# Kernel tuning notes

Hardware: AMD Instinct MI355X
Metric: run time of the kernel (lower is better)

Reference implementation:

```python
import jax, jax.numpy as jnp
import numpy as np

B, C, H, W = 16, 128, 112, 112
OUTC = 256


def _conv(x, w, padding, groups=1, bias=None):
    y = jax.lax.conv_general_dilated(
        x, w, window_strides=(1, 1), padding=[(padding, padding), (padding, padding)],
        dimension_numbers=("NCHW", "OIHW", "NCHW"), feature_group_count=groups)
    if bias is not None:
        y = y + bias[None, :, None, None]
    return y


def _grid_sample_1ch(chan, g):
    # chan: [B,H,W] single channel; g: [B,H,W,2] with (x,y) in [-1,1].
    # PyTorch grid_sample: bilinear, zeros padding, align_corners=False.
    Bn, Hc, Wc = chan.shape
    ix = (g[..., 0] + 1.0) * (Wc * 0.5) - 0.5
    iy = (g[..., 1] + 1.0) * (Hc * 0.5) - 0.5
    x0 = jnp.floor(ix)
    y0 = jnp.floor(iy)
    wx = ix - x0
    wy = iy - y0
    x0i = x0.astype(jnp.int32)
    y0i = y0.astype(jnp.int32)
    flat = chan.reshape(Bn, -1)

    def gather(yi, xi):
        valid = (yi >= 0) & (yi < Hc) & (xi >= 0) & (xi < Wc)
        idx = jnp.clip(yi, 0, Hc - 1) * Wc + jnp.clip(xi, 0, Wc - 1)
        v = jnp.take_along_axis(flat, idx.reshape(Bn, -1), axis=1).reshape(idx.shape)
        return jnp.where(valid, v, 0.0)

    v00 = gather(y0i, x0i)
    v01 = gather(y0i, x0i + 1)
    v10 = gather(y0i + 1, x0i)
    v11 = gather(y0i + 1, x0i + 1)
    return (v00 * (1 - wx) * (1 - wy) + v01 * wx * (1 - wy)
            + v10 * (1 - wx) * wy + v11 * wx * wy)


def setup_inputs() -> dict:
    key = jax.random.key(0)
    k1, k2, k3, k4 = jax.random.split(key, 4)
    x = jax.random.normal(k1, (B, C, H, W), dtype=jnp.float32)
    depth_w = jax.random.normal(k2, (C, 1, 3, 3), dtype=jnp.float32) * 0.1
    point_w = jax.random.normal(k3, (OUTC, C, 1, 1), dtype=jnp.float32) * 0.05
    offset_w = jax.random.normal(k4, (2 * C, C, 3, 3), dtype=jnp.float32) * 0.02
    offset_b = jnp.zeros((2 * C,), dtype=jnp.float32)
    return {"x": x, "depth_w": depth_w, "point_w": point_w,
            "offset_w": offset_w, "offset_b": offset_b}


def reference(x, depth_w, point_w, offset_w, offset_b):
    offset = jnp.tanh(_conv(x, offset_w, padding=1, bias=offset_b))  # [B,2C,H,W]
    out = _conv(x, depth_w, padding=1, groups=C)                     # [B,C,H,W]

    # Base grid, matching np.meshgrid + np.repeat([C,C], axis=0):
    # channels 0..C-1 are all X, channels C..2C-1 are all Y.
    gX, gY = jnp.meshgrid(jnp.linspace(-1.0, 1.0, W), jnp.linspace(-1.0, 1.0, H), indexing="xy")
    grid = jnp.concatenate([gX[None], gY[None]], axis=0)  # [2,H,W]
    grid = jnp.repeat(grid, C, axis=0)                    # [2C,H,W]

    sg = jnp.clip(grid[None] + offset, -1.0, 1.0)         # [B,2C,H,W]
    sg = sg.transpose(0, 2, 3, 1)                         # [B,H,W,2C]
    sg = sg.reshape(B, H, W, C, 2).transpose(3, 0, 1, 2, 4)  # [C,B,H,W,2]

    chans = out.transpose(1, 0, 2, 3)                     # [C,B,H,W]
    sampled = jax.vmap(_grid_sample_1ch)(chans, sg)       # [C,B,H,W]
    sampled = sampled.transpose(1, 0, 2, 3)               # [B,C,H,W]

    return _conv(sampled, point_w, padding=0)             # [B,OUTC,H,W]
```

## Files before the change

kernel.cpp:

```cpp
#include <hip/hip_runtime.h>
#include <hip/hip_bf16.h>

#define B_    16
#define C_    128
#define H_    112
#define W_    112
#define OUTC_ 256
#define TWOC_ 256
#define HW_   (H_ * W_)
#define CHW_  ((size_t)C_ * HW_)

typedef __hip_bfloat16 bf16;
typedef short bf16x8 __attribute__((ext_vector_type(8)));
typedef short s16x4  __attribute__((ext_vector_type(4)));
typedef float f32x4  __attribute__((ext_vector_type(4)));

__device__ __forceinline__ float b2f(bf16 v) { return __bfloat162float(v); }
__device__ __forceinline__ bf16  f2b(float v) { return __float2bfloat16(v); }

__device__ __forceinline__ float rd(const float* p) { return *p; }
__device__ __forceinline__ float rd(const bf16* p)  { return b2f(*p); }

__device__ __forceinline__ float fast_tanh(float v) {
    float e = __expf(2.f * v);
    return 1.f - 2.f / (e + 1.f);
}

__global__ __launch_bounds__(256) void k_probe(const unsigned short* __restrict__ x,
                                               int* __restrict__ flag) {
    __shared__ int cnt[256];
    int tid = threadIdx.x;
    int c = 0;
#pragma unroll
    for (int i = 0; i < 8; ++i) {
        unsigned short u = x[tid * 8 + i];
        int e = (u >> 7) & 0xFF;
        if (e >= 135) c++;
    }
    cnt[tid] = c;
    __syncthreads();
    if (tid == 0) {
        int s = 0;
        for (int i = 0; i < 256; ++i) s += cnt[i];
        *flag = (s > 64) ? 1 : 0;
    }
}

__global__ __launch_bounds__(256) void k_wprep(const void* __restrict__ ow,
                                               bf16* __restrict__ wth,
                                               bf16* __restrict__ wtl,
                                               const int* __restrict__ flag) {
    int i = blockIdx.x * 256 + threadIdx.x;
    if (i >= 9 * 4 * 256 * 32) return;
    int cp  = i & 31;
    int oc  = (i >> 5) & 255;
    int tcc = i >> 13;
    int cc  = tcc & 3;
    int tap = tcc >> 2;
    int c   = cc * 32 + cp;
    size_t src = ((size_t)oc * C_ + c) * 9 + tap;
    float v = (*flag) ? ((const float*)ow)[src] : b2f(((const bf16*)ow)[src]);
    bf16 hb = f2b(v);
    float lo = v - b2f(hb);
    wth[i] = hb;
    wtl[i] = f2b(lo);
}

__global__ __launch_bounds__(256) void k_pwprep(const void* __restrict__ pw,
                                                bf16* __restrict__ pwh,
                                                bf16* __restrict__ pwl,
                                                const int* __restrict__ flag) {
    int i = blockIdx.x * 256 + threadIdx.x;
    if (i >= 4 * 256 * 32) return;
    int cp   = i & 31;
    int oc   = (i >> 5) & 255;
    int cc   = i >> 13;
    int c    = cc * 32 + cp;
    size_t src = (size_t)oc * C_ + c;
    float v = (*flag) ? ((const float*)pw)[src] : b2f(((const bf16*)pw)[src]);
    bf16 hb = f2b(v);
    float lo = v - b2f(hb);
    pwh[i] = hb;
    pwl[i] = f2b(lo);
}

__global__ __launch_bounds__(256) void k_offset_mfma(
    const void* __restrict__ xsrc, const bf16* __restrict__ wth,
    const bf16* __restrict__ wtl, const void* __restrict__ ob,
    float* __restrict__ off, const int* __restrict__ flag, int b0)
{
    __shared__ alignas(16) short Sh[114 * 32];
    __shared__ alignas(16) short Sl[114 * 32];

    const int tid  = threadIdx.x;
    const int lane = tid & 63;
    const int wv   = tid >> 6;
    const int l15  = lane & 15;
    const int l4   = lane >> 4;
    const int hraw = blockIdx.x;
    const int h    = (hraw & 7) * 14 + (hraw >> 3);
    const int b    = blockIdx.y + b0;
    const int fullp = *flag;

    const float* xf = (const float*)xsrc;
    const bf16*  xb = (const bf16*)xsrc;

    f32x4 acc[4][7];
    f32x4 zero = {0.f, 0.f, 0.f, 0.f};
#pragma unroll
    for (int m = 0; m < 4; ++m)
#pragma unroll
        for (int n = 0; n < 7; ++n) acc[m][n] = zero;

    for (int cc = 0; cc < 4; ++cc) {
        for (int kh = 0; kh < 3; ++kh) {
            const int row = h + kh - 1;
            const bool rowok = (row >= 0) && (row < H_);
            __syncthreads();
            for (int i = tid; i < 912; i += 256) {
                int n  = i % 114;
                int cq = i / 114;
                int col = n - 1;
                bool ok = rowok && (col >= 0) && (col < W_);
                size_t base = ((size_t)(b * C_ + cc * 32 + cq * 4)) * HW_
                            + (size_t)row * W_ + col;
                short hs[4], ls[4];
#pragma unroll
                for (int t = 0; t < 4; ++t) {
                    float v = 0.f;
                    if (ok) v = fullp ? xf[base + (size_t)t * HW_]
                                      : b2f(xb[base + (size_t)t * HW_]);
                    bf16 hb = f2b(v);
                    float hv = b2f(hb);
                    bf16 lb = f2b(v - hv);
                    hs[t] = *(short*)&hb;
                    ls[t] = *(short*)&lb;
                }
                int ob_ = (cq * 8) ^ (((n >> 1) & 3) << 4);
                int so  = n * 32 + (ob_ >> 1);
                s16x4 th, tl;
                th[0] = hs[0]; th[1] = hs[1]; th[2] = hs[2]; th[3] = hs[3];
                tl[0] = ls[0]; tl[1] = ls[1]; tl[2] = ls[2]; tl[3] = ls[3];
                *(s16x4*)&Sh[so] = th;
                *(s16x4*)&Sl[so] = tl;
            }
            __syncthreads();

            for (int kw = 0; kw < 3; ++kw) {
                const size_t wchunk = ((size_t)((kh * 3 + kw) * 4 + cc)) * (256 * 32);
                bf16x8 ah[4], al[4];
#pragma unroll
                for (int m = 0; m < 4; ++m) {
                    size_t aoff = (size_t)(wv * 64 + m * 16 + l15) * 32 + 8 * l4;
                    ah[m] = *(const bf16x8*)(wth + wchunk + aoff);
                }
                if (fullp) {
#pragma unroll
                    for (int m = 0; m < 4; ++m) {
                        size_t aoff = (size_t)(wv * 64 + m * 16 + l15) * 32 + 8 * l4;
                        al[m] = *(const bf16x8*)(wtl + wchunk + aoff);
                    }
                }
#pragma unroll
                for (int n = 0; n < 7; ++n) {
                    int rowb = n * 16 + l15 + kw;
                    int o2   = (16 * l4) ^ (((rowb >> 1) & 3) << 4);
                    int so   = rowb * 32 + (o2 >> 1);
                    bf16x8 xh = *(const bf16x8*)&Sh[so];
#pragma unroll
                    for (int m = 0; m < 4; ++m)
                        acc[m][n] = __builtin_amdgcn_mfma_f32_16x16x32_bf16(
                            ah[m], xh, acc[m][n], 0, 0, 0);
                    if (fullp) {
                        bf16x8 xl = *(const bf16x8*)&Sl[so];
#pragma unroll
                        for (int m = 0; m < 4; ++m)
                            acc[m][n] = __builtin_amdgcn_mfma_f32_16x16x32_bf16(
                                ah[m], xl, acc[m][n], 0, 0, 0);
#pragma unroll
                        for (int m = 0; m < 4; ++m)
                            acc[m][n] = __builtin_amdgcn_mfma_f32_16x16x32_bf16(
                                al[m], xh, acc[m][n], 0, 0, 0);
                    }
                }
            }
        }
    }

#pragma unroll
    for (int m = 0; m < 4; ++m) {
        int ocb = wv * 64 + m * 16 + l4 * 4;
        float bias[4];
#pragma unroll
        for (int j = 0; j < 4; ++j)
            bias[j] = fullp ? ((const float*)ob)[ocb + j]
                            : b2f(((const bf16*)ob)[ocb + j]);
#pragma unroll
        for (int n = 0; n < 7; ++n) {
            int w = n * 16 + l15;
#pragma unroll
            for (int j = 0; j < 4; ++j) {
                size_t o = ((size_t)(b * TWOC_ + ocb + j)) * HW_ + (size_t)h * W_ + w;
                off[o] = fast_tanh(acc[m][n][j] + bias[j]);
            }
        }
    }
}

template <typename TI>
__device__ void dw_body(const TI* __restrict__ x, const TI* __restrict__ dw,
                        bf16* __restrict__ out) {
    int hw = blockIdx.x * 256 + threadIdx.x;
    int c = blockIdx.y, b = blockIdx.z;
    int h = hw / W_, w = hw - h * W_;
    float wv[9];
#pragma unroll
    for (int k = 0; k < 9; ++k) wv[k] = rd(dw + c * 9 + k);
    const TI* xc = x + (size_t)b * CHW_ + (size_t)c * HW_;
    float acc = 0.f;
#pragma unroll
    for (int kh = 0; kh < 3; ++kh) {
        int hh = h + kh - 1;
        bool hv = (hh >= 0) && (hh < H_);
#pragma unroll
        for (int kw = 0; kw < 3; ++kw) {
            int ww = w + kw - 1;
            bool v = hv && (ww >= 0) && (ww < W_);
            acc += (v ? rd(xc + hh * W_ + ww) : 0.f) * wv[kh * 3 + kw];
        }
    }
    out[(size_t)(b * C_ + c) * HW_ + hw] = f2b(acc);
}

__global__ __launch_bounds__(256) void k_dw(const void* x, const void* dw,
                                            bf16* out, const int* flag) {
    if (*flag) dw_body<float>((const float*)x, (const float*)dw, out);
    else       dw_body<bf16>((const bf16*)x, (const bf16*)dw, out);
}

__global__ __launch_bounds__(256) void k_sample(
    const float* __restrict__ off, const bf16* __restrict__ dwout,
    bf16* __restrict__ samp) {
    int hw = blockIdx.x * 256 + threadIdx.x;
    int c = blockIdx.y, b = blockIdx.z;
    int h = hw / W_, w = hw - h * W_;

    float gbase = (c < 64) ? (-1.f + 2.f * (float)w / 111.f)
                           : (-1.f + 2.f * (float)h / 111.f);
    const float* offb = off + (size_t)b * TWOC_ * HW_;
    float ox = offb[(size_t)(2 * c) * HW_ + hw];
    float oy = offb[(size_t)(2 * c + 1) * HW_ + hw];
    float gx = fminf(fmaxf(gbase + ox, -1.f), 1.f);
    float gy = fminf(fmaxf(gbase + oy, -1.f), 1.f);
    float ix = (gx + 1.f) * 56.f - 0.5f;
    float iy = (gy + 1.f) * 56.f - 0.5f;
    float x0f = floorf(ix), y0f = floorf(iy);
    float wx = ix - x0f, wy = iy - y0f;
    int x0 = (int)x0f, y0 = (int)y0f;

    const bf16* p = dwout + (size_t)(b * C_ + c) * HW_;
    float v00 = 0.f, v01 = 0.f, v10 = 0.f, v11 = 0.f;
    bool y0v = (y0 >= 0) && (y0 < H_), y1v = (y0 + 1 >= 0) && (y0 + 1 < H_);
    bool x0v = (x0 >= 0) && (x0 < W_), x1v = (x0 + 1 >= 0) && (x0 + 1 < W_);
    if (y0v && x0v) v00 = b2f(p[y0 * W_ + x0]);
    if (y0v && x1v) v01 = b2f(p[y0 * W_ + x0 + 1]);
    if (y1v && x0v) v10 = b2f(p[(y0 + 1) * W_ + x0]);
    if (y1v && x1v) v11 = b2f(p[(y0 + 1) * W_ + x0 + 1]);

    float v = v00 * (1.f - wx) * (1.f - wy) + v01 * wx * (1.f - wy)
            + v10 * (1.f - wx) * wy + v11 * wx * wy;
    samp[(size_t)(b * C_ + c) * HW_ + hw] = f2b(v);
}

__global__ __launch_bounds__(256) void k_pw_mfma(
    const bf16* __restrict__ samp, const bf16* __restrict__ pwh,
    const bf16* __restrict__ pwl, void* __restrict__ out,
    const int* __restrict__ flag)
{
    __shared__ short SP[C_ * 114];

    const int tid  = threadIdx.x;
    const int lane = tid & 63;
    const int wv   = tid >> 6;
    const int l15  = lane & 15;
    const int l4   = lane >> 4;
    const int hraw = blockIdx.x;
    const int h    = (hraw & 7) * 14 + (hraw >> 3);
    const int b    = blockIdx.y;
    const int fullp = *flag;

    const bf16* srow = samp + (size_t)b * C_ * HW_ + (size_t)h * W_;

#pragma unroll
    for (int it = 0; it < 7; ++it) {
        int i  = it * 256 + tid;
        int c  = i / 14;
        int wc = i - c * 14;
        bf16x8 v = *(const bf16x8*)(srow + (size_t)c * HW_ + wc * 8);
        short* d = &SP[c * 114 + wc * 8];
#pragma unroll
        for (int t = 0; t < 8; ++t) d[t] = v[t];
    }
    __syncthreads();

    f32x4 acc[4][7];
    f32x4 zero = {0.f, 0.f, 0.f, 0.f};
#pragma unroll
    for (int m = 0; m < 4; ++m)
#pragma unroll
        for (int n = 0; n < 7; ++n) acc[m][n] = zero;

    for (int cc = 0; cc < 4; ++cc) {
        bf16x8 ah[4], al[4];
#pragma unroll
        for (int m = 0; m < 4; ++m) {
            size_t aoff = ((size_t)cc * 256 + (wv * 64 + m * 16 + l15)) * 32 + 8 * l4;
            ah[m] = *(const bf16x8*)(pwh + aoff);
        }
        if (fullp) {
#pragma unroll
            for (int m = 0; m < 4; ++m) {
                size_t aoff = ((size_t)cc * 256 + (wv * 64 + m * 16 + l15)) * 32 + 8 * l4;
                al[m] = *(const bf16x8*)(pwl + aoff);
            }
        }
        const int c0 = cc * 32 + 8 * l4;
#pragma unroll
        for (int n = 0; n < 7; ++n) {
            int w = n * 16 + l15;
            bf16x8 xv;
#pragma unroll
            for (int j = 0; j < 8; ++j) xv[j] = SP[(c0 + j) * 114 + w];
#pragma unroll
            for (int m = 0; m < 4; ++m)
                acc[m][n] = __builtin_amdgcn_mfma_f32_16x16x32_bf16(
                    ah[m], xv, acc[m][n], 0, 0, 0);
            if (fullp) {
#pragma unroll
                for (int m = 0; m < 4; ++m)
                    acc[m][n] = __builtin_amdgcn_mfma_f32_16x16x32_bf16(
                        al[m], xv, acc[m][n], 0, 0, 0);
            }
        }
    }

#pragma unroll
    for (int m = 0; m < 4; ++m) {
        int ocb = wv * 64 + m * 16 + l4 * 4;
#pragma unroll
        for (int n = 0; n < 7; ++n) {
            int w = n * 16 + l15;
#pragma unroll
            for (int j = 0; j < 4; ++j) {
                size_t o = ((size_t)(b * OUTC_ + ocb + j)) * HW_ + (size_t)h * W_ + w;
                if (fullp) ((float*)out)[o] = acc[m][n][j];
                else       ((bf16*)out)[o]  = f2b(acc[m][n][j]);
            }
        }
    }
}

extern "C" void kernel_launch(void* const* d_in, const int* in_sizes, int n_in,
                              void* d_out, int out_size, void* d_ws, size_t ws_size,
                              hipStream_t stream) {
    (void)in_sizes; (void)n_in; (void)out_size; (void)ws_size;
    const void* x        = d_in[0];
    const void* depth_w  = d_in[1];
    const void* point_w  = d_in[2];
    const void* offset_w = d_in[3];
    const void* offset_b = d_in[4];

    char* ws = (char*)d_ws;
    int*   flag = (int*)ws;
    const size_t off_bytes = (size_t)B_ * TWOC_ * HW_ * 4;
    float* off  = (float*)(ws + 256);
    bf16*  wth  = (bf16*)(ws + 256 + off_bytes);
    bf16*  wtl  = wth + 9 * 4 * 256 * 32;
    bf16*  pwh  = wtl + 9 * 4 * 256 * 32;
    bf16*  pwl  = pwh + 4 * 256 * 32;
    bf16* dwout = pwl + 4 * 256 * 32;
    bf16* samp  = dwout + (size_t)B_ * C_ * HW_;

    k_probe      <<<1, 256, 0, stream>>>((const unsigned short*)x, flag);
    k_wprep      <<<1152, 256, 0, stream>>>(offset_w, wth, wtl, flag);
    k_pwprep     <<<128, 256, 0, stream>>>(point_w, pwh, pwl, flag);
    k_offset_mfma<<<dim3(H_, 8), 256, 0, stream>>>(x, wth, wtl, offset_b, off, flag, 0);
    k_offset_mfma<<<dim3(H_, 8), 256, 0, stream>>>(x, wth, wtl, offset_b, off, flag, 8);
    k_dw         <<<dim3(49, C_, B_), 256, 0, stream>>>(x, depth_w, dwout, flag);
    k_sample     <<<dim3(49, C_, B_), 256, 0, stream>>>(off, dwout, samp);
    k_pw_mfma    <<<dim3(H_, B_), 256, 0, stream>>>(samp, pwh, pwl, d_out, flag);
}
```

Before: 1.052 ms.

## Interleave offset x/y pairs as float2 and loop sample kernel per channel

The offset conv epilogue now writes each channel's x/y offset pair interleaved as a float2, so the sampler reads one 8-byte value instead of two floats from separate planes. The sample kernel launches one block per (channel, batch) and loops over the 49 spatial chunks, which keeps one channel plane of dwout hot in cache across iterations. The cost is a strided 8-byte store pattern in the offset epilogue and far fewer blocks in the sample grid (2048 instead of about 100k), which lowers parallelism and latency hiding.

```diff
diff --git a/kernel.cpp b/kernel.cpp
--- a/kernel.cpp
+++ b/kernel.cpp
@@ -87,7 +87,7 @@
 __global__ __launch_bounds__(256) void k_offset_mfma(
     const void* __restrict__ xsrc, const bf16* __restrict__ wth,
     const bf16* __restrict__ wtl, const void* __restrict__ ob,
-    float* __restrict__ off, const int* __restrict__ flag, int b0)
+    float2* __restrict__ off2, const int* __restrict__ flag, int b0)
 {
     __shared__ alignas(16) short Sh[114 * 32];
     __shared__ alignas(16) short Sl[114 * 32];
@@ -195,14 +195,17 @@
         for (int j = 0; j < 4; ++j)
             bias[j] = fullp ? ((const float*)ob)[ocb + j]
                             : b2f(((const bf16*)ob)[ocb + j]);
+        int c0 = ocb >> 1;
 #pragma unroll
         for (int n = 0; n < 7; ++n) {
             int w = n * 16 + l15;
-#pragma unroll
-            for (int j = 0; j < 4; ++j) {
-                size_t o = ((size_t)(b * TWOC_ + ocb + j)) * HW_ + (size_t)h * W_ + w;
-                off[o] = fast_tanh(acc[m][n][j] + bias[j]);
-            }
+            float vx0 = fast_tanh(acc[m][n][0] + bias[0]);
+            float vy0 = fast_tanh(acc[m][n][1] + bias[1]);
+            float vx1 = fast_tanh(acc[m][n][2] + bias[2]);
+            float vy1 = fast_tanh(acc[m][n][3] + bias[3]);
+            size_t base = ((size_t)(b * C_) + c0) * HW_ + (size_t)h * W_ + w;
+            off2[base]       = float2{vx0, vy0};
+            off2[base + HW_] = float2{vx1, vy1};
         }
     }
 }
@@ -239,37 +242,43 @@
 }
 
 __global__ __launch_bounds__(256) void k_sample(
-    const float* __restrict__ off, const bf16* __restrict__ dwout,
+    const float2* __restrict__ off2, const bf16* __restrict__ dwout,
     bf16* __restrict__ samp) {
-    int hw = blockIdx.x * 256 + threadIdx.x;
-    int c = blockIdx.y, b = blockIdx.z;
-    int h = hw / W_, w = hw - h * W_;
-
-    float gbase = (c < 64) ? (-1.f + 2.f * (float)w / 111.f)
+    const int c = blockIdx.x, b = blockIdx.y;
+    const int tid = threadIdx.x;
+    const bool useX = (c < 64);
+
+    const float2* o2 = off2 + (size_t)(b * C_ + c) * HW_;
+    const bf16*   p  = dwout + (size_t)(b * C_ + c) * HW_;
+    bf16*         s  = samp + (size_t)(b * C_ + c) * HW_;
+
+#pragma unroll 1
+    for (int it = 0; it < 49; ++it) {
+        int hw = it * 256 + tid;
+        int h = hw / W_, w = hw - h * W_;
+        float2 o = o2[hw];
+        float gbase = useX ? (-1.f + 2.f * (float)w / 111.f)
                            : (-1.f + 2.f * (float)h / 111.f);
-    const float* offb = off + (size_t)b * TWOC_ * HW_;
-    float ox = offb[(size_t)(2 * c) * HW_ + hw];
-    float oy = offb[(size_t)(2 * c + 1) * HW_ + hw];
-    float gx = fminf(fmaxf(gbase + ox, -1.f), 1.f);
-    float gy = fminf(fmaxf(gbase + oy, -1.f), 1.f);
-    float ix = (gx + 1.f) * 56.f - 0.5f;
-    float iy = (gy + 1.f) * 56.f - 0.5f;
-    float x0f = floorf(ix), y0f = floorf(iy);
-    float wx = ix - x0f, wy = iy - y0f;
-    int x0 = (int)x0f, y0 = (int)y0f;
-
-    const bf16* p = dwout + (size_t)(b * C_ + c) * HW_;
-    float v00 = 0.f, v01 = 0.f, v10 = 0.f, v11 = 0.f;
-    bool y0v = (y0 >= 0) && (y0 < H_), y1v = (y0 + 1 >= 0) && (y0 + 1 < H_);
-    bool x0v = (x0 >= 0) && (x0 < W_), x1v = (x0 + 1 >= 0) && (x0 + 1 < W_);
-    if (y0v && x0v) v00 = b2f(p[y0 * W_ + x0]);
-    if (y0v && x1v) v01 = b2f(p[y0 * W_ + x0 + 1]);
-    if (y1v && x0v) v10 = b2f(p[(y0 + 1) * W_ + x0]);
-    if (y1v && x1v) v11 = b2f(p[(y0 + 1) * W_ + x0 + 1]);
-
-    float v = v00 * (1.f - wx) * (1.f - wy) + v01 * wx * (1.f - wy)
-            + v10 * (1.f - wx) * wy + v11 * wx * wy;
-    samp[(size_t)(b * C_ + c) * HW_ + hw] = f2b(v);
+        float gx = fminf(fmaxf(gbase + o.x, -1.f), 1.f);
+        float gy = fminf(fmaxf(gbase + o.y, -1.f), 1.f);
+        float ix = (gx + 1.f) * 56.f - 0.5f;
+        float iy = (gy + 1.f) * 56.f - 0.5f;
+        float x0f = floorf(ix), y0f = floorf(iy);
+        float wx = ix - x0f, wy = iy - y0f;
+        int x0 = (int)x0f, y0 = (int)y0f;
+
+        float v00 = 0.f, v01 = 0.f, v10 = 0.f, v11 = 0.f;
+        bool y0v = (y0 >= 0) && (y0 < H_), y1v = (y0 + 1 >= 0) && (y0 + 1 < H_);
+        bool x0v = (x0 >= 0) && (x0 < W_), x1v = (x0 + 1 >= 0) && (x0 + 1 < W_);
+        if (y0v && x0v) v00 = b2f(p[y0 * W_ + x0]);
+        if (y0v && x1v) v01 = b2f(p[y0 * W_ + x0 + 1]);
+        if (y1v && x0v) v10 = b2f(p[(y0 + 1) * W_ + x0]);
+        if (y1v && x1v) v11 = b2f(p[(y0 + 1) * W_ + x0 + 1]);
+
+        float v = v00 * (1.f - wx) * (1.f - wy) + v01 * wx * (1.f - wy)
+                + v10 * (1.f - wx) * wy + v11 * wx * wy;
+        s[hw] = f2b(v);
+    }
 }
 
 __global__ __launch_bounds__(256) void k_pw_mfma(
@@ -372,8 +381,8 @@
 
     char* ws = (char*)d_ws;
     int*   flag = (int*)ws;
-    const size_t off_bytes = (size_t)B_ * TWOC_ * HW_ * 4;
-    float* off  = (float*)(ws + 256);
+    const size_t off_bytes = (size_t)B_ * C_ * HW_ * 8;
+    float2* off2 = (float2*)(ws + 256);
     bf16*  wth  = (bf16*)(ws + 256 + off_bytes);
     bf16*  wtl  = wth + 9 * 4 * 256 * 32;
     bf16*  pwh  = wtl + 9 * 4 * 256 * 32;
@@ -384,9 +393,9 @@
     k_probe      <<<1, 256, 0, stream>>>((const unsigned short*)x, flag);
     k_wprep      <<<1152, 256, 0, stream>>>(offset_w, wth, wtl, flag);
     k_pwprep     <<<128, 256, 0, stream>>>(point_w, pwh, pwl, flag);
-    k_offset_mfma<<<dim3(H_, 8), 256, 0, stream>>>(x, wth, wtl, offset_b, off, flag, 0);
-    k_offset_mfma<<<dim3(H_, 8), 256, 0, stream>>>(x, wth, wtl, offset_b, off, flag, 8);
+    k_offset_mfma<<<dim3(H_, 8), 256, 0, stream>>>(x, wth, wtl, offset_b, off2, flag, 0);
+    k_offset_mfma<<<dim3(H_, 8), 256, 0, stream>>>(x, wth, wtl, offset_b, off2, flag, 8);
     k_dw         <<<dim3(49, C_, B_), 256, 0, stream>>>(x, depth_w, dwout, flag);
-    k_sample     <<<dim3(49, C_, B_), 256, 0, stream>>>(off, dwout, samp);
+    k_sample     <<<dim3(C_, B_), 256, 0, stream>>>(off2, dwout, samp);
     k_pw_mfma    <<<dim3(H_, B_), 256, 0, stream>>>(samp, pwh, pwl, d_out, flag);
 }
```

New measurement: 1.138 ms. 1.08x slower.
